# Kernel optimization log

Measured on AMD Instinct MI355X. Metric: run time of the kernel, lower is better.

## Reference

```python
import jax, jax.numpy as jnp
import numpy as np

HIDDEN = 5120
HEAD_DIM = 128
HQ = 40
HKV = 8
NUM_MOD = 3
Q_SIZE = HQ * HEAD_DIM          # 5120
KV_SIZE = HKV * HEAD_DIM        # 1024
GATE = HQ                       # attn gating enabled
QKV_OUT = Q_SIZE + 2 * KV_SIZE + GATE  # 7208
EPS = 1e-6
N_TOK = 2048


def setup_inputs() -> dict:
    key = jax.random.key(0)
    ks = jax.random.split(key, 8)
    s = 0.02
    return {
        "hidden_states": jax.random.normal(ks[0], (N_TOK, HIDDEN), jnp.float32),
        "rope": jax.random.normal(ks[1], (N_TOK, HEAD_DIM), jnp.float32),
        "pre_norm_w": jax.random.normal(ks[2], (NUM_MOD * HIDDEN,), jnp.float32) * s,
        "qkv_w": jax.random.normal(ks[3], (NUM_MOD * QKV_OUT, HIDDEN), jnp.float32) * s,
        "q_norm_w": jax.random.normal(ks[4], (NUM_MOD * HEAD_DIM,), jnp.float32) * s,
        "k_norm_w": jax.random.normal(ks[5], (NUM_MOD * HEAD_DIM,), jnp.float32) * s,
        "proj_w": jax.random.normal(ks[6], (NUM_MOD * HIDDEN, Q_SIZE), jnp.float32) * s,
        "modality_ids": jax.random.randint(ks[7], (N_TOK,), 0, NUM_MOD, jnp.int64),
    }


def _mm_rmsnorm(x, w_flat, mids, dim):
    # per-token modality weight slice; residual parameterization (w + 1)
    w = w_flat.reshape(NUM_MOD, dim)[mids]  # [N, dim]
    if x.ndim == 3:
        w = w[:, None, :]  # broadcast over heads
    rms = jax.lax.rsqrt(jnp.mean(x * x, axis=-1, keepdims=True) + EPS)
    return x * rms * (w + 1.0)


def _moe_linear(x, w_flat, mids, out_f):
    # 3 GEMMs (one per expert), then per-token select -- same math as masked dispatch
    wm = w_flat.reshape(NUM_MOD, out_f, x.shape[-1])
    outs = jnp.einsum('nd,mod->nmo', x, wm)  # [N, 3, out_f]
    return jnp.take_along_axis(outs, mids[:, None, None], axis=1)[:, 0, :]


def _rotary(x, cos, sin):
    # x: [N, H, D]; cos/sin: [N, D/2]
    x1, x2 = jnp.split(x, 2, axis=-1)
    c = cos[:, None, :]
    s = sin[:, None, :]
    return jnp.concatenate([x1 * c - x2 * s, x1 * s + x2 * c], axis=-1)


def reference(hidden_states, rope, pre_norm_w, qkv_w, q_norm_w, k_norm_w, proj_w, modality_ids):
    N = hidden_states.shape[0]
    mids = modality_ids

    h = _mm_rmsnorm(hidden_states, pre_norm_w, mids, HIDDEN)
    qkv = _moe_linear(h, qkv_w, mids, QKV_OUT)  # [N, 7208]
    q, k, v, g = jnp.split(qkv, [Q_SIZE, Q_SIZE + KV_SIZE, Q_SIZE + 2 * KV_SIZE], axis=-1)
    q = q.reshape(N, HQ, HEAD_DIM)
    k = k.reshape(N, HKV, HEAD_DIM)
    v = v.reshape(N, HKV, HEAD_DIM)

    q = _mm_rmsnorm(q, q_norm_w, mids, HEAD_DIM)
    k = _mm_rmsnorm(k, k_norm_w, mids, HEAD_DIM)

    sin, cos = jnp.split(rope, 2, axis=-1)  # rope.chunk(2, dim=-1) -> sin, cos
    q = _rotary(q, cos, sin)
    k = _rotary(k, cos, sin)

    # GQA attention over the full token sequence
    G = HQ // HKV
    qg = q.reshape(N, HKV, G, HEAD_DIM)
    scale = 1.0 / np.sqrt(HEAD_DIM).astype(np.float32)
    scores = jnp.einsum('nkgd,mkd->kgnm', qg, k) * scale  # [8, 5, N, N]
    p = jax.nn.softmax(scores, axis=-1)
    o = jnp.einsum('kgnm,mkd->nkgd', p, v).reshape(N, HQ, HEAD_DIM)

    o = o * jax.nn.sigmoid(g)[:, :, None]  # attention gating per q-head
    o = o.reshape(N, Q_SIZE)
    return _moe_linear(o, proj_w, mids, HIDDEN)
```

## Files before the change

### kernel.cpp

```cpp
#include <hip/hip_runtime.h>
#include <hip/hip_bf16.h>

#define N_TOK 2048
#define HIDDEN 5120
#define HEAD_DIM 128
#define HQ 40
#define HKV 8
#define QKV_OUT 7208
#define Q_SIZE 5120
#define KV_SIZE 1024

typedef __attribute__((ext_vector_type(8))) short bf16x8;
typedef __attribute__((ext_vector_type(4))) float f32x4;
typedef __attribute__((ext_vector_type(4))) unsigned short us4;

__device__ inline unsigned short f2bf(float f) {
    return __builtin_bit_cast(unsigned short, __float2bfloat16(f));
}
__device__ inline float bf2f(unsigned short s) {
    unsigned u = ((unsigned)s) << 16;
    return __builtin_bit_cast(float, u);
}
__device__ inline f32x4 mfma16(bf16x8 a, bf16x8 b, f32x4 c) {
    return __builtin_amdgcn_mfma_f32_16x16x32_bf16(a, b, c, 0, 0, 0);
}
__device__ inline void gl16(const void* g, void* l) {
    __builtin_amdgcn_global_load_lds((__attribute__((address_space(1))) void*)g,
                                     (__attribute__((address_space(3))) void*)l, 16, 0, 0);
}

__global__ void k_sort(const int* __restrict__ mids_raw, int* __restrict__ meta,
                       int* __restrict__ perm) {
    int l = threadIdx.x;
    int oddnz = 0;
    for (int c = 0; c < 32; ++c) {
        int idx = c * 64 + l;
        int v = mids_raw[idx];
        if ((idx & 1) && v != 0) oddnz = 1;
    }
    bool is64 = (__ballot(oddnz) == 0ULL);
    int c0 = 0, c1 = 0;
    for (int c = 0; c < 32; ++c) {
        int i = c * 64 + l;
        int m = is64 ? mids_raw[2 * i] : mids_raw[i];
        c0 += (m == 0); c1 += (m == 1);
    }
    for (int o = 32; o; o >>= 1) { c0 += __shfl_xor(c0, o); c1 += __shfl_xor(c1, o); }
    if (l == 0) { meta[0] = 0; meta[1] = c0; meta[2] = c0 + c1; meta[3] = N_TOK; }
    int r0 = 0, r1 = c0, r2 = c0 + c1;
    unsigned long long below = (1ULL << l) - 1ULL;
    for (int c = 0; c < 32; ++c) {
        int i = c * 64 + l;
        int m = is64 ? mids_raw[2 * i] : mids_raw[i];
        unsigned long long b0 = __ballot(m == 0), b1 = __ballot(m == 1), b2 = __ballot(m == 2);
        int pos = (m == 0) ? r0 + __popcll(b0 & below)
                : (m == 1) ? r1 + __popcll(b1 & below)
                           : r2 + __popcll(b2 & below);
        perm[pos] = i;
        r0 += __popcll(b0); r1 += __popcll(b1); r2 += __popcll(b2);
    }
}

__global__ __launch_bounds__(256) void k_prenorm(const float* __restrict__ hidden,
        const float* __restrict__ pnw, const int* __restrict__ meta,
        const int* __restrict__ perm, unsigned short* __restrict__ h) {
    int i = blockIdx.x;
    int m = (i >= meta[1]) + (i >= meta[2]);
    int t = perm[i];
    const float4* x = (const float4*)(hidden + (size_t)t * HIDDEN);
    const float4* wv = (const float4*)(pnw + (size_t)m * HIDDEN);
    int tid = threadIdx.x;
    float4 xv[5];
    float ss = 0.f;
#pragma unroll
    for (int j = 0; j < 5; ++j) {
        xv[j] = x[tid + j * 256];
        ss += xv[j].x * xv[j].x + xv[j].y * xv[j].y + xv[j].z * xv[j].z + xv[j].w * xv[j].w;
    }
    for (int o = 32; o; o >>= 1) ss += __shfl_xor(ss, o);
    __shared__ float red[4];
    if ((tid & 63) == 0) red[tid >> 6] = ss;
    __syncthreads();
    float rms = rsqrtf((red[0] + red[1] + red[2] + red[3]) * (1.f / HIDDEN) + 1e-6f);
    us4* dst = (us4*)(h + (size_t)i * HIDDEN);
#pragma unroll
    for (int j = 0; j < 5; ++j) {
        float4 w = wv[tid + j * 256];
        us4 o4;
        o4.x = f2bf(xv[j].x * rms * (w.x + 1.f));
        o4.y = f2bf(xv[j].y * rms * (w.y + 1.f));
        o4.z = f2bf(xv[j].z * rms * (w.z + 1.f));
        o4.w = f2bf(xv[j].w * rms * (w.w + 1.f));
        dst[tid + j * 256] = o4;
    }
}

template <int NOUT, bool SCATTER>
__global__ __launch_bounds__(256, 2) void k_gemm(
        const unsigned short* __restrict__ A, const float* __restrict__ Bw,
        unsigned short* __restrict__ outB, float* __restrict__ outF,
        const int* __restrict__ meta, const int* __restrict__ perm,
        int nx, int ny) {
    int nwg = nx * ny * 3;
    int bid = blockIdx.x;
    int xcd = bid & 7, o = bid >> 3;
    int q = nwg >> 3, r = nwg & 7;
    int swz = (xcd < r ? xcd * (q + 1) : r * (q + 1) + (xcd - r) * q) + o;
    int mz = swz / (nx * ny);
    int rest = swz - mz * (nx * ny);
    int ty = rest / nx, tx = rest - ty * nx;

    int rowS = meta[mz], rowE = meta[mz + 1];
    int row0 = rowS + tx * 128;
    if (row0 >= rowE) return;
    int col0 = ty * 128;
    const float* Bm = Bw + (size_t)mz * NOUT * HIDDEN;

    __shared__ __align__(16) char smem[65536];
    int tid = threadIdx.x, l = tid & 63, w = tid >> 6;
    int wr = (w >> 1) * 64, wc = (w & 1) * 64;

    f32x4 acc[4][4] = {};

    const int lr = l >> 3, lc = l & 7;
    const int sch = (lc ^ lr) * 8;
    const unsigned short* ag[4];
#pragma unroll
    for (int j = 0; j < 4; ++j) {
        int ar = row0 + 32 * j + 8 * w + lr;
        if (ar > rowE - 1) ar = rowE - 1;
        ag[j] = A + (size_t)ar * HIDDEN + sch;
    }
    const float* bg[4];
    int brow[4];
#pragma unroll
    for (int j = 0; j < 4; ++j) {
        int bc = col0 + 32 * j + 8 * w + lr;
        if (bc > NOUT - 1) bc = NOUT - 1;
        bg[j] = Bm + (size_t)bc * HIDDEN + lc * 8;
        brow[j] = 32 * j + 8 * w + lr;
    }
    char* asw = smem + w * 1024;

    float4 breg[4][2];
    auto STAGE = [&](int buf, int kk) {
#pragma unroll
        for (int j = 0; j < 4; ++j) gl16(ag[j] + kk, asw + buf * 32768 + j * 4096);
#pragma unroll
        for (int j = 0; j < 4; ++j) {
            breg[j][0] = *(const float4*)(bg[j] + kk);
            breg[j][1] = *(const float4*)(bg[j] + kk + 4);
        }
    };
    auto BWRITE = [&](int buf) {
#pragma unroll
        for (int j = 0; j < 4; ++j) {
            bf16x8 pk;
            pk[0] = (short)f2bf(breg[j][0].x); pk[1] = (short)f2bf(breg[j][0].y);
            pk[2] = (short)f2bf(breg[j][0].z); pk[3] = (short)f2bf(breg[j][0].w);
            pk[4] = (short)f2bf(breg[j][1].x); pk[5] = (short)f2bf(breg[j][1].y);
            pk[6] = (short)f2bf(breg[j][1].z); pk[7] = (short)f2bf(breg[j][1].w);
            int row = brow[j];
            *(bf16x8*)(smem + buf * 32768 + 16384 + row * 128 +
                       ((lc * 16) ^ ((row & 7) << 4))) = pk;
        }
    };
    auto COMPUTE = [&](int buf) {
        char* baseA = smem + buf * 32768;
        char* baseB = baseA + 16384;
#pragma unroll
        for (int ks = 0; ks < 2; ++ks) {
            bf16x8 af[4], bfm[4];
#pragma unroll
            for (int mi = 0; mi < 4; ++mi) {
                int row = wr + mi * 16 + (l & 15);
                af[mi] = *(const bf16x8*)(baseA + row * 128 +
                            ((ks * 64 + (l >> 4) * 16) ^ ((row & 7) << 4)));
            }
#pragma unroll
            for (int ni = 0; ni < 4; ++ni) {
                int row = wc + ni * 16 + (l & 15);
                bfm[ni] = *(const bf16x8*)(baseB + row * 128 +
                            ((ks * 64 + (l >> 4) * 16) ^ ((row & 7) << 4)));
            }
#pragma unroll
            for (int mi = 0; mi < 4; ++mi)
#pragma unroll
                for (int ni = 0; ni < 4; ++ni)
                    acc[mi][ni] = mfma16(af[mi], bfm[ni], acc[mi][ni]);
        }
    };

    STAGE(0, 0);
    BWRITE(0);
    asm volatile("s_waitcnt vmcnt(0) lgkmcnt(0)" ::: "memory");
    __builtin_amdgcn_sched_barrier(0);
    __builtin_amdgcn_s_barrier();
    __builtin_amdgcn_sched_barrier(0);
    int cur = 0;
#pragma unroll 1
    for (int kt = 0; kt < HIDDEN / 64 - 1; ++kt) {
        STAGE(cur ^ 1, (kt + 1) * 64);
        COMPUTE(cur);
        BWRITE(cur ^ 1);
        asm volatile("s_waitcnt vmcnt(0) lgkmcnt(0)" ::: "memory");
        __builtin_amdgcn_sched_barrier(0);
        __builtin_amdgcn_s_barrier();
        __builtin_amdgcn_sched_barrier(0);
        cur ^= 1;
    }
    COMPUTE(cur);

#pragma unroll
    for (int mi = 0; mi < 4; ++mi) {
        int rbase = row0 + wr + mi * 16 + ((l >> 4) << 2);
#pragma unroll
        for (int ni = 0; ni < 4; ++ni) {
            int col = col0 + wc + ni * 16 + (l & 15);
            if (col >= NOUT) continue;
#pragma unroll
            for (int rr = 0; rr < 4; ++rr) {
                int row = rbase + rr;
                if (row >= rowE) continue;
                if (SCATTER) {
                    int t = perm[row];
                    outF[(size_t)t * HIDDEN + col] = acc[mi][ni][rr];
                } else {
                    outB[(size_t)row * NOUT + col] = f2bf(acc[mi][ni][rr]);
                }
            }
        }
    }
}

__global__ __launch_bounds__(256) void k_qknorm(const unsigned short* __restrict__ qkv,
        const float* __restrict__ rope, const float* __restrict__ qnw,
        const float* __restrict__ knw, const int* __restrict__ meta,
        const int* __restrict__ perm, unsigned short* __restrict__ qb,
        unsigned short* __restrict__ kb, float* __restrict__ gate) {
    int i = blockIdx.x;
    int m = (i >= meta[1]) + (i >= meta[2]);
    int t = perm[i];
    int tid = threadIdx.x, w = tid >> 6, l = tid & 63;
    const unsigned short* base = qkv + (size_t)i * QKV_OUT;
    const float* rp = rope + (size_t)t * HEAD_DIM;
    const float qscale = 0.08838834764831845f * 1.4426950408889634f;
    for (int hh = w; hh < 48; hh += 4) {
        bool isq = hh < 40;
        const unsigned short* src = base + (isq ? hh * 128 : Q_SIZE + (hh - 40) * 128);
        float x0 = bf2f(src[2 * l]), x1 = bf2f(src[2 * l + 1]);
        float ss = x0 * x0 + x1 * x1;
        for (int o = 32; o; o >>= 1) ss += __shfl_xor(ss, o);
        float rms = rsqrtf(ss * (1.f / 128.f) + 1e-6f);
        const float* nw = (isq ? qnw : knw) + m * 128;
        float y0 = x0 * rms * (nw[2 * l] + 1.f);
        float y1 = x1 * rms * (nw[2 * l + 1] + 1.f);
        float p0 = __shfl_xor(y0, 32);
        float p1 = __shfl_xor(y1, 32);
        float r0v, r1v;
        if (l < 32) {
            int d = 2 * l;
            r0v = y0 * rp[64 + d] - p0 * rp[d];
            r1v = y1 * rp[64 + d + 1] - p1 * rp[d + 1];
        } else {
            int d = 2 * l - 64;
            r0v = p0 * rp[d] + y0 * rp[64 + d];
            r1v = p1 * rp[d + 1] + y1 * rp[64 + d + 1];
        }
        if (isq) {
            r0v *= qscale; r1v *= qscale;
            unsigned short* dst = qb + (size_t)i * Q_SIZE + hh * 128 + 2 * l;
            dst[0] = f2bf(r0v); dst[1] = f2bf(r1v);
        } else {
            unsigned short* dst = kb + (size_t)i * KV_SIZE + (hh - 40) * 128 + 2 * l;
            dst[0] = f2bf(r0v); dst[1] = f2bf(r1v);
        }
    }
    if (tid < HQ) {
        float g = bf2f(base[Q_SIZE + 2 * KV_SIZE + tid]);
        gate[(size_t)i * HQ + tid] = 1.f / (1.f + expf(-g));
    }
}

__global__ __launch_bounds__(256) void k_vtrans(const unsigned short* __restrict__ qkv,
                                                unsigned short* __restrict__ vT) {
    int t0 = blockIdx.x * 64, db = blockIdx.y * 64, kvh = blockIdx.z;
    __shared__ unsigned short tile[64][68];
    int tid = threadIdx.x;
    int tr = tid >> 2, seg = tid & 3;
    const unsigned short* src = qkv + (size_t)(t0 + tr) * QKV_OUT + Q_SIZE + KV_SIZE +
                                kvh * 128 + db + seg * 16;
    us4* drow = (us4*)&tile[tr][seg * 16];
#pragma unroll
    for (int q = 0; q < 4; ++q) drow[q] = ((const us4*)src)[q];
    __syncthreads();
    int dr = tid >> 2;
    unsigned short* dst = vT + ((size_t)kvh * 128 + db + dr) * N_TOK + t0 + seg * 16;
    unsigned short buf[16];
#pragma unroll
    for (int j = 0; j < 16; ++j) buf[j] = tile[seg * 16 + j][dr];
#pragma unroll
    for (int q = 0; q < 4; ++q) ((us4*)dst)[q] = ((us4*)buf)[q];
}

__global__ __launch_bounds__(256) void k_attn(
        const unsigned short* __restrict__ qb,
        const unsigned short* __restrict__ kb,
        const unsigned short* __restrict__ vT,
        const float* __restrict__ gate,
        unsigned short* __restrict__ og) {
    int qt = blockIdx.x, qh = blockIdx.y, kvh = qh / 5;
    int tid = threadIdx.x, w = tid >> 6, l = tid & 63;
    int q0 = qt * 128 + w * 32;
    __shared__ __align__(16) char smem[49152];
    char* Ks = smem;
    char* Vs = smem + 16384;
    char* Ps = smem + 32768 + w * 4096;

    bf16x8 qf[2][4];
#pragma unroll
    for (int mi = 0; mi < 2; ++mi)
#pragma unroll
        for (int ks = 0; ks < 4; ++ks)
            qf[mi][ks] = *(const bf16x8*)(qb + (size_t)(q0 + mi * 16 + (l & 15)) * Q_SIZE +
                                          qh * 128 + ks * 32 + (l >> 4) * 8);

    f32x4 oacc[2][8] = {};
    f32x4 psum[2] = {};

    int kr = tid >> 2, kseg = tid & 3;
    int vr = tid >> 1, vh2 = tid & 1;

#pragma unroll 1
    for (int kt = 0; kt < 32; ++kt) {
        int t0 = kt * 64;
        bf16x8 kv4[4], vv4[4];
        const unsigned short* ksrc = kb + (size_t)(t0 + kr) * KV_SIZE + kvh * 128 + kseg * 32;
        const unsigned short* vsrc = vT + ((size_t)kvh * 128 + vr) * N_TOK + t0 + vh2 * 32;
#pragma unroll
        for (int q = 0; q < 4; ++q) {
            kv4[q] = *(const bf16x8*)(ksrc + q * 8);
            vv4[q] = *(const bf16x8*)(vsrc + q * 8);
        }
        __syncthreads();
#pragma unroll
        for (int q = 0; q < 4; ++q) {
            *(bf16x8*)(Ks + kr * 256 + ((((kseg * 4 + q) * 16)) ^ ((kr & 7) << 4))) = kv4[q];
            *(bf16x8*)(Vs + vr * 128 + ((((vh2 * 4 + q) * 16)) ^ ((vr & 7) << 4))) = vv4[q];
        }
        __syncthreads();
        f32x4 s[2][4] = {};
#pragma unroll
        for (int ks = 0; ks < 4; ++ks) {
            bf16x8 kf[4];
#pragma unroll
            for (int ni = 0; ni < 4; ++ni) {
                int row = ni * 16 + (l & 15);
                kf[ni] = *(const bf16x8*)(Ks + row * 256 +
                            ((ks * 64 + (l >> 4) * 16) ^ ((row & 7) << 4)));
            }
#pragma unroll
            for (int mi = 0; mi < 2; ++mi)
#pragma unroll
                for (int ni = 0; ni < 4; ++ni)
                    s[mi][ni] = mfma16(qf[mi][ks], kf[ni], s[mi][ni]);
        }
#pragma unroll
        for (int mi = 0; mi < 2; ++mi)
#pragma unroll
            for (int ni = 0; ni < 4; ++ni) {
#pragma unroll
                for (int r = 0; r < 4; ++r) {
                    float p = exp2f(s[mi][ni][r]);
                    psum[mi][r] += p;
                    int qr = mi * 16 + ((l >> 4) << 2) + r;
                    int tcb = (ni * 16 + (l & 15)) * 2;
                    *(unsigned short*)(Ps + qr * 128 +
                        (tcb ^ (((qr >> 2) & 3) << 5))) = f2bf(p);
                }
            }
#pragma unroll
        for (int ks = 0; ks < 2; ++ks) {
            bf16x8 pa[2];
#pragma unroll
            for (int mi = 0; mi < 2; ++mi) {
                int qr = mi * 16 + (l & 15);
                pa[mi] = *(const bf16x8*)(Ps + qr * 128 +
                            ((ks * 64 + (l >> 4) * 16) ^ (((qr >> 2) & 3) << 5)));
            }
#pragma unroll
            for (int nd = 0; nd < 8; ++nd) {
                int row = nd * 16 + (l & 15);
                bf16x8 vf = *(const bf16x8*)(Vs + row * 128 +
                            ((ks * 64 + (l >> 4) * 16) ^ ((row & 7) << 4)));
#pragma unroll
                for (int mi = 0; mi < 2; ++mi)
                    oacc[mi][nd] = mfma16(pa[mi], vf, oacc[mi][nd]);
            }
        }
    }
#pragma unroll
    for (int mi = 0; mi < 2; ++mi)
#pragma unroll
        for (int r = 0; r < 4; ++r) {
            float v = psum[mi][r];
            v += __shfl_xor(v, 1);
            v += __shfl_xor(v, 2);
            v += __shfl_xor(v, 4);
            v += __shfl_xor(v, 8);
            psum[mi][r] = v;
        }
#pragma unroll
    for (int mi = 0; mi < 2; ++mi)
#pragma unroll
        for (int r = 0; r < 4; ++r) {
            int row = q0 + mi * 16 + ((l >> 4) << 2) + r;
            float sc = (1.f / psum[mi][r]) * gate[(size_t)row * HQ + qh];
#pragma unroll
            for (int nd = 0; nd < 8; ++nd)
                og[(size_t)row * Q_SIZE + qh * 128 + nd * 16 + (l & 15)] =
                    f2bf(oacc[mi][nd][r] * sc);
        }
}

extern "C" void kernel_launch(void* const* d_in, const int* in_sizes, int n_in,
                              void* d_out, int out_size, void* d_ws, size_t ws_size,
                              hipStream_t stream) {
    const float* hidden = (const float*)d_in[0];
    const float* rope   = (const float*)d_in[1];
    const float* pnw    = (const float*)d_in[2];
    const float* qkvw   = (const float*)d_in[3];
    const float* qnw    = (const float*)d_in[4];
    const float* knw    = (const float*)d_in[5];
    const float* projw  = (const float*)d_in[6];
    const int*   mids   = (const int*)d_in[7];
    float* out = (float*)d_out;

    char* ws = (char*)d_ws;
    const size_t small_bytes = 16384 +
        (size_t)N_TOK * HIDDEN * 2 +
        (size_t)N_TOK * QKV_OUT * 2 +
        (size_t)N_TOK * Q_SIZE * 2 +
        (size_t)N_TOK * KV_SIZE * 2 +
        (size_t)N_TOK * KV_SIZE * 2 +
        (size_t)N_TOK * Q_SIZE * 2 +
        (size_t)N_TOK * HQ * 4;
    if (ws_size < small_bytes) return;

    int* meta = (int*)ws;
    int* perm = (int*)(ws + 64);
    unsigned short* h   = (unsigned short*)(ws + 16384);
    unsigned short* qkv = h   + (size_t)N_TOK * HIDDEN;
    unsigned short* qb  = qkv + (size_t)N_TOK * QKV_OUT;
    unsigned short* kb  = qb  + (size_t)N_TOK * Q_SIZE;
    unsigned short* vT  = kb  + (size_t)N_TOK * KV_SIZE;
    unsigned short* og  = vT  + (size_t)N_TOK * KV_SIZE;
    float* gate = (float*)(og + (size_t)N_TOK * Q_SIZE);

    k_sort<<<1, 64, 0, stream>>>(mids, meta, perm);
    k_prenorm<<<2048, 256, 0, stream>>>(hidden, pnw, meta, perm, h);
    k_gemm<QKV_OUT, false><<<16 * 57 * 3, 256, 0, stream>>>(
        h, qkvw, qkv, nullptr, meta, perm, 16, 57);
    k_qknorm<<<2048, 256, 0, stream>>>(qkv, rope, qnw, knw, meta, perm, qb, kb, gate);
    k_vtrans<<<dim3(32, 2, 8), 256, 0, stream>>>(qkv, vT);
    k_attn<<<dim3(16, 40), 256, 0, stream>>>(qb, kb, vT, gate, og);
    k_gemm<HIDDEN, true><<<16 * 40 * 3, 256, 0, stream>>>(
        og, projw, nullptr, out, meta, perm, 16, 40);
}
```

Before: 927.2 us.

## Enlarge GEMM tile to 256x128 with 512 threads and triple-buffered LDS pipeline

Both MoE GEMMs now use 512-thread blocks computing 256-row by 128-column tiles, so each fp32 weight tile is loaded and converted to bf16 once for twice as many rows. The k-loop moves from double to triple buffering in dynamic LDS (about 144 KB), using partial vmcnt waits so one stage's global loads stay in flight while the current one is computed. The cost is a single block per CU because of the LDS footprint, and a larger wasted tail for modality segments that do not fill 256 rows.

Measured after the change: 928.2 us. Within noise of the previous version (+0.1%).

```diff
diff --git a/kernel.cpp b/kernel.cpp
--- a/kernel.cpp
+++ b/kernel.cpp
@@ -96,11 +96,12 @@
 }
 
 template <int NOUT, bool SCATTER>
-__global__ __launch_bounds__(256, 2) void k_gemm(
+__global__ __launch_bounds__(512, 2) void k_gemm(
         const unsigned short* __restrict__ A, const float* __restrict__ Bw,
         unsigned short* __restrict__ outB, float* __restrict__ outF,
         const int* __restrict__ meta, const int* __restrict__ perm,
         int nx, int ny) {
+    extern __shared__ char smem[];
     int nwg = nx * ny * 3;
     int bid = blockIdx.x;
     int xcd = bid & 7, o = bid >> 3;
@@ -111,12 +112,11 @@
     int ty = rest / nx, tx = rest - ty * nx;
 
     int rowS = meta[mz], rowE = meta[mz + 1];
-    int row0 = rowS + tx * 128;
+    int row0 = rowS + tx * 256;
     if (row0 >= rowE) return;
     int col0 = ty * 128;
     const float* Bm = Bw + (size_t)mz * NOUT * HIDDEN;
 
-    __shared__ __align__(16) char smem[65536];
     int tid = threadIdx.x, l = tid & 63, w = tid >> 6;
     int wr = (w >> 1) * 64, wc = (w & 1) * 64;
 
@@ -127,47 +127,47 @@
     const unsigned short* ag[4];
 #pragma unroll
     for (int j = 0; j < 4; ++j) {
-        int ar = row0 + 32 * j + 8 * w + lr;
+        int ar = row0 + 64 * j + 8 * w + lr;
         if (ar > rowE - 1) ar = rowE - 1;
         ag[j] = A + (size_t)ar * HIDDEN + sch;
     }
-    const float* bg[4];
-    int brow[4];
-#pragma unroll
-    for (int j = 0; j < 4; ++j) {
-        int bc = col0 + 32 * j + 8 * w + lr;
+    const float* bg[2];
+    int brow[2];
+#pragma unroll
+    for (int j = 0; j < 2; ++j) {
+        int bc = col0 + 64 * j + 8 * w + lr;
         if (bc > NOUT - 1) bc = NOUT - 1;
         bg[j] = Bm + (size_t)bc * HIDDEN + lc * 8;
-        brow[j] = 32 * j + 8 * w + lr;
-    }
-    char* asw = smem + w * 1024;
-
-    float4 breg[4][2];
-    auto STAGE = [&](int buf, int kk) {
-#pragma unroll
-        for (int j = 0; j < 4; ++j) gl16(ag[j] + kk, asw + buf * 32768 + j * 4096);
-#pragma unroll
-        for (int j = 0; j < 4; ++j) {
-            breg[j][0] = *(const float4*)(bg[j] + kk);
-            breg[j][1] = *(const float4*)(bg[j] + kk + 4);
-        }
+        brow[j] = 64 * j + 8 * w + lr;
+    }
+
+    float4 bregA[2][2], bregB[2][2];
+    auto STAGE = [&](float4 (&br)[2][2], int buf, int kk) {
+        char* ab = smem + buf * 49152 + w * 1024;
+#pragma unroll
+        for (int j = 0; j < 4; ++j) gl16(ag[j] + kk, ab + j * 8192);
+#pragma unroll
+        for (int j = 0; j < 2; ++j) {
+            br[j][0] = *(const float4*)(bg[j] + kk);
+            br[j][1] = *(const float4*)(bg[j] + kk + 4);
+        }
+        __builtin_amdgcn_sched_barrier(0);
     };
-    auto BWRITE = [&](int buf) {
-#pragma unroll
-        for (int j = 0; j < 4; ++j) {
+    auto BWRITE = [&](float4 (&br)[2][2], int buf) {
+#pragma unroll
+        for (int j = 0; j < 2; ++j) {
             bf16x8 pk;
-            pk[0] = (short)f2bf(breg[j][0].x); pk[1] = (short)f2bf(breg[j][0].y);
-            pk[2] = (short)f2bf(breg[j][0].z); pk[3] = (short)f2bf(breg[j][0].w);
-            pk[4] = (short)f2bf(breg[j][1].x); pk[5] = (short)f2bf(breg[j][1].y);
-            pk[6] = (short)f2bf(breg[j][1].z); pk[7] = (short)f2bf(breg[j][1].w);
-            int row = brow[j];
-            *(bf16x8*)(smem + buf * 32768 + 16384 + row * 128 +
-                       ((lc * 16) ^ ((row & 7) << 4))) = pk;
+            pk[0] = (short)f2bf(br[j][0].x); pk[1] = (short)f2bf(br[j][0].y);
+            pk[2] = (short)f2bf(br[j][0].z); pk[3] = (short)f2bf(br[j][0].w);
+            pk[4] = (short)f2bf(br[j][1].x); pk[5] = (short)f2bf(br[j][1].y);
+            pk[6] = (short)f2bf(br[j][1].z); pk[7] = (short)f2bf(br[j][1].w);
+            *(bf16x8*)(smem + buf * 49152 + 32768 + brow[j] * 128 +
+                       ((lc * 16) ^ ((brow[j] & 7) << 4))) = pk;
         }
     };
     auto COMPUTE = [&](int buf) {
-        char* baseA = smem + buf * 32768;
-        char* baseB = baseA + 16384;
+        char* baseA = smem + buf * 49152;
+        char* baseB = baseA + 32768;
 #pragma unroll
         for (int ks = 0; ks < 2; ++ks) {
             bf16x8 af[4], bfm[4];
@@ -191,25 +191,31 @@
         }
     };
 
-    STAGE(0, 0);
-    BWRITE(0);
-    asm volatile("s_waitcnt vmcnt(0) lgkmcnt(0)" ::: "memory");
-    __builtin_amdgcn_sched_barrier(0);
-    __builtin_amdgcn_s_barrier();
-    __builtin_amdgcn_sched_barrier(0);
-    int cur = 0;
-#pragma unroll 1
-    for (int kt = 0; kt < HIDDEN / 64 - 1; ++kt) {
-        STAGE(cur ^ 1, (kt + 1) * 64);
-        COMPUTE(cur);
-        BWRITE(cur ^ 1);
-        asm volatile("s_waitcnt vmcnt(0) lgkmcnt(0)" ::: "memory");
+    int bufc = 0;
+    auto BODY = [&](float4 (&br)[2][2], int stage_kt, bool last) {
+        if (last) asm volatile("s_waitcnt vmcnt(0)" ::: "memory");
+        else      asm volatile("s_waitcnt vmcnt(8)" ::: "memory");
+        __builtin_amdgcn_sched_barrier(0);
+        BWRITE(br, bufc);
+        asm volatile("s_waitcnt lgkmcnt(0)" ::: "memory");
         __builtin_amdgcn_sched_barrier(0);
         __builtin_amdgcn_s_barrier();
         __builtin_amdgcn_sched_barrier(0);
-        cur ^= 1;
-    }
-    COMPUTE(cur);
+        COMPUTE(bufc);
+        if (stage_kt < HIDDEN / 64) {
+            int bs = bufc + 2; if (bs >= 3) bs -= 3;
+            STAGE(br, bs, stage_kt * 64);
+        }
+        bufc = (bufc + 1 == 3) ? 0 : bufc + 1;
+    };
+
+    STAGE(bregA, 0, 0);
+    STAGE(bregB, 1, 64);
+#pragma unroll 1
+    for (int kt = 0; kt < HIDDEN / 64; kt += 2) {
+        BODY(bregA, kt + 2, false);
+        BODY(bregB, kt + 3, kt + 3 >= HIDDEN / 64);
+    }
 
 #pragma unroll
     for (int mi = 0; mi < 4; ++mi) {
@@ -457,13 +463,19 @@
     unsigned short* og  = vT  + (size_t)N_TOK * KV_SIZE;
     float* gate = (float*)(og + (size_t)N_TOK * Q_SIZE);
 
+    const int LDS3 = 3 * 49152;
+    hipFuncSetAttribute(reinterpret_cast<const void*>(k_gemm<QKV_OUT, false>),
+                        hipFuncAttributeMaxDynamicSharedMemorySize, LDS3);
+    hipFuncSetAttribute(reinterpret_cast<const void*>(k_gemm<HIDDEN, true>),
+                        hipFuncAttributeMaxDynamicSharedMemorySize, LDS3);
+
     k_sort<<<1, 64, 0, stream>>>(mids, meta, perm);
     k_prenorm<<<2048, 256, 0, stream>>>(hidden, pnw, meta, perm, h);
-    k_gemm<QKV_OUT, false><<<16 * 57 * 3, 256, 0, stream>>>(
-        h, qkvw, qkv, nullptr, meta, perm, 16, 57);
+    k_gemm<QKV_OUT, false><<<8 * 57 * 3, 512, LDS3, stream>>>(
+        h, qkvw, qkv, nullptr, meta, perm, 8, 57);
     k_qknorm<<<2048, 256, 0, stream>>>(qkv, rope, qnw, knw, meta, perm, qb, kb, gate);
     k_vtrans<<<dim3(32, 2, 8), 256, 0, stream>>>(qkv, vT);
     k_attn<<<dim3(16, 40), 256, 0, stream>>>(qb, kb, vT, gate, og);
-    k_gemm<HIDDEN, true><<<16 * 40 * 3, 256, 0, stream>>>(
-        og, projw, nullptr, out, meta, perm, 16, 40);
-}
+    k_gemm<HIDDEN, true><<<8 * 40 * 3, 512, LDS3, stream>>>(
+        og, projw, nullptr, out, meta, perm, 8, 40);
+}
```
